# Kernel tuning notes

Hardware: AMD Instinct MI355X
Metric: run time of the kernel (lower is better)

The kernel has to match this reference:

```python
import jax, jax.numpy as jnp
from jax import lax
import numpy as np

H = 128          # hidden_dim
VOCAB = 200000   # word_dim
L = 32           # words per node
NUM_LEAVES = 2048
NUM_PARENTS = 2047
MAXC = 4         # max child slots in a tree row
NCLASS = 4


def setup_inputs() -> dict:
    key = jax.random.key(0)
    ks = jax.random.split(key, 16)
    N = NUM_LEAVES + NUM_PARENTS
    x_word = jax.random.uniform(ks[0], (N, L), dtype=jnp.float32)
    x_index = jax.random.randint(ks[1], (N, L), 0, VOCAB)
    # caterpillar tree: parent idx has one leaf child and the previous parent
    idx = np.arange(NUM_PARENTS)
    tree = np.full((NUM_PARENTS, MAXC), -1, dtype=np.int32)
    tree[:, 0] = idx
    tree[:, 1] = np.where(idx > 0, NUM_LEAVES + idx - 1, NUM_LEAVES - 1)
    tree = jnp.asarray(tree)
    y = jax.random.uniform(ks[2], (NCLASS,), dtype=jnp.float32)
    def init(k, shp):
        return 0.1 * jax.random.normal(k, shp, dtype=jnp.float32)
    return dict(
        x_word=x_word, x_index=x_index, tree=tree, y=y,
        E_bu=init(ks[3], (H, VOCAB)),
        WQ=init(ks[4], (H, H)), WK=init(ks[5], (H, H)), WV=init(ks[6], (H, H)),
        W_z=init(ks[7], (H, H)), U_z=init(ks[8], (H, H)), b_z=jnp.zeros((H,), jnp.float32),
        W_r=init(ks[9], (H, H)), U_r=init(ks[10], (H, H)), b_r=jnp.zeros((H,), jnp.float32),
        W_h=init(ks[11], (H, H)), U_h=init(ks[12], (H, H)), b_h=jnp.zeros((H,), jnp.float32),
        W_out=init(ks[13], (NCLASS, H)), b_out=jnp.zeros((NCLASS,), jnp.float32),
    )


def _forward(x_word, y, E_bu, WQ, WK, WV, W_z, U_z, b_z, W_r, U_r, b_r,
             W_h, U_h, b_h, W_out, b_out, x_index, tree):
    Hd = E_bu.shape[0]
    # parent_xe for every node: weighted sum of embedding columns  [N, H]
    emb = E_bu.T[x_index]                        # [N, L, H] gather
    xe = jnp.einsum('nlh,nl->nh', emb, x_word)
    n_parents = tree.shape[0]
    n_leaves = x_word.shape[0] - n_parents

    def cell(xe_i, h_tilde):
        # W.mul(v).sum(dim=1) == W @ v in the torch code
        z = jax.nn.sigmoid(W_z @ xe_i + U_z @ h_tilde + b_z)
        r = jax.nn.sigmoid(W_r @ xe_i + U_r @ h_tilde + b_r)
        c = jnp.tanh(W_h @ xe_i + U_h @ (h_tilde * r) + b_h)
        return z * h_tilde + (1.0 - z) * c

    # leaves: child_h == 0  =>  h_tilde == 0 (vectorized over all leaves)
    xe_leaf = xe[:n_leaves]
    z_l = jax.nn.sigmoid(xe_leaf @ W_z.T + b_z)
    c_l = jnp.tanh(xe_leaf @ W_h.T + b_h)
    leaf_h = (1.0 - z_l) * c_l

    node_h0 = jnp.zeros((x_word.shape[0], Hd), xe.dtype).at[:n_leaves].set(leaf_h)
    scale = 1.0 / jnp.sqrt(jnp.asarray(Hd, xe.dtype))

    def step(node_h, inp):
        xe_p, row, i = inp
        mask = row >= 0
        child_h = node_h[jnp.clip(row, 0)]                  # [MAXC, H]
        query = jax.nn.sigmoid(xe_p @ WQ)                   # sigmoid(xe @ WQ)
        keyv = child_h @ WK
        val = child_h @ WV
        scores = jnp.where(mask, (query * scale * keyv).sum(-1), -1e9)
        attn = jax.nn.softmax(scores)                       # over children
        h_tilde = attn @ val
        h = cell(xe_p, h_tilde)
        return node_h.at[i].set(h), h

    idxs = jnp.arange(n_parents) + n_leaves
    _, parent_hs = lax.scan(step, node_h0, (xe[n_leaves:], tree, idxs))
    root = parent_hs[-1]
    pred = jax.nn.softmax(W_out @ root + b_out)
    loss = jnp.sum((y - pred) ** 2)
    return pred, loss


def reference(x_word, x_index, tree, y, E_bu, WQ, WK, WV, W_z, U_z, b_z,
              W_r, U_r, b_r, W_h, U_h, b_h, W_out, b_out):
    return _forward(x_word, y, E_bu, WQ, WK, WV, W_z, U_z, b_z, W_r, U_r, b_r,
                    W_h, U_h, b_h, W_out, b_out, x_index, tree)
```

## Files before the change

### kernel.cpp

```cpp
#include <hip/hip_runtime.h>
#include <math.h>

#define HD 128
#define LW 32
#define VOCABN 200000
#define NLEAF 2048
#define NPAR 2047
#define NNODE 4095
#define MAXC 4
#define NCLASS 4
#define SCALE 0.08838834764831845f

#define OFF_XE   0
#define OFF_NODE 524160
#define OFF_W3   786304
#define OFF_WQ   851840
#define OFF_AZ   1113856
#define OFF_AR   1375872
#define OFF_AH   1637888
#define OFF_PREV 1899904
#define OFF_ES   2685952
#define OFF_HG   2688000
#define OFF_HTR  2688128
#define OFF_ET   2688256
#define WS_END   (OFF_ET + (size_t)VOCABN * HD)

#define BARL() asm volatile("s_waitcnt lgkmcnt(0)\n\ts_barrier" ::: "memory")
#define PIN4(v) asm volatile("" : "+v"((v).x), "+v"((v).y), "+v"((v).z), "+v"((v).w))
#define LD4(p, k) (*(const float4*)((p) + 4 * (k)))

#define PIN_ALL() do { PIN4(A0); PIN4(A1); PIN4(A2); PIN4(A3); \
    PIN4(A4); PIN4(A5); PIN4(A6); PIN4(A7); PIN4(A8); PIN4(A9); \
    PIN4(A10); PIN4(A11); PIN4(A12); PIN4(A13); PIN4(A14); PIN4(A15); } while (0)

#define CHRL(W, B) { \
    float s0_ = __int_as_float(__builtin_amdgcn_readlane(xi_, (B) + 0)); \
    float s1_ = __int_as_float(__builtin_amdgcn_readlane(xi_, (B) + 1)); \
    float s2_ = __int_as_float(__builtin_amdgcn_readlane(xi_, (B) + 2)); \
    float s3_ = __int_as_float(__builtin_amdgcn_readlane(xi_, (B) + 3)); \
    a0 += (W).x * s0_ + (W).y * s1_; a1 += (W).z * s2_ + (W).w * s3_; }

#define MATVEC_RL() do { \
    CHRL(A0, 0)   CHRL(A1, 4)   CHRL(A2, 8)   CHRL(A3, 12) \
    CHRL(A4, 16)  CHRL(A5, 20)  CHRL(A6, 24)  CHRL(A7, 28) \
    CHRL(A8, 32)  CHRL(A9, 36)  CHRL(A10, 40) CHRL(A11, 44) \
    CHRL(A12, 48) CHRL(A13, 52) CHRL(A14, 56) CHRL(A15, 60) } while (0)

__global__ void k_xe(const float* __restrict__ xw, const int* __restrict__ xi,
                     const float* __restrict__ E, float* __restrict__ xe) {
    int n = blockIdx.x;
    int h = threadIdx.x;
    __shared__ int   sidx[LW];
    __shared__ float sw[LW];
    if (h < LW) { sidx[h] = xi[n * LW + h]; sw[h] = xw[n * LW + h]; }
    __syncthreads();
    float acc = 0.f;
#pragma unroll
    for (int l = 0; l < LW; ++l)
        acc += E[(size_t)h * VOCABN + sidx[l]] * sw[l];
    xe[(size_t)n * HD + h] = acc;
}

__global__ void k_transpose(const float* __restrict__ E, float* __restrict__ ET) {
    __shared__ float tile[32][33];
    int vb = blockIdx.x * 32, hb = blockIdx.y * 32;
    int tx = threadIdx.x, ty = threadIdx.y;
#pragma unroll
    for (int r = 0; r < 32; r += 8)
        tile[ty + r][tx] = E[(size_t)(hb + ty + r) * VOCABN + vb + tx];
    __syncthreads();
#pragma unroll
    for (int r = 0; r < 32; r += 8)
        ET[(size_t)(vb + ty + r) * HD + hb + tx] = tile[tx][ty + r];
}

__global__ void k_xe_t(const float* __restrict__ xw, const int* __restrict__ xi,
                       const float* __restrict__ ET, float* __restrict__ xe) {
    int n = blockIdx.x;
    int h = threadIdx.x;
    __shared__ int   sidx[LW];
    __shared__ float sw[LW];
    if (h < LW) { sidx[h] = xi[n * LW + h]; sw[h] = xw[n * LW + h]; }
    __syncthreads();
    float acc = 0.f;
#pragma unroll
    for (int l = 0; l < LW; ++l)
        acc += ET[(size_t)sidx[l] * HD + h] * sw[l];
    xe[(size_t)n * HD + h] = acc;
}

__global__ void k_leaf(const float* __restrict__ xe, const float* __restrict__ Wz,
                       const float* __restrict__ bz, const float* __restrict__ Wh,
                       const float* __restrict__ bh, float* __restrict__ node_h) {
    int n = blockIdx.x;
    int j = threadIdx.x;
    __shared__ float xl[HD];
    xl[j] = xe[(size_t)n * HD + j];
    __syncthreads();
    float az = bz[j], ah = bh[j];
    const float* wzr = Wz + (size_t)j * HD;
    const float* whr = Wh + (size_t)j * HD;
#pragma unroll 4
    for (int k = 0; k < HD; ++k) { az += wzr[k] * xl[k]; ah += whr[k] * xl[k]; }
    float z = 1.f / (1.f + expf(-az));
    float c = tanhf(ah);
    node_h[(size_t)n * HD + j] = (1.f - z) * c;
}

__global__ void k_fuse(const float* __restrict__ WV, const float* __restrict__ Uz,
                       const float* __restrict__ Ur, const float* __restrict__ Uh,
                       float* __restrict__ w3) {
    int r = blockIdx.x;
    int b = threadIdx.x;
    float v;
    if (r < 128) {
        v = WV[(size_t)b * HD + r];
    } else if (r < 384) {
        const float* u  = (r < 256 ? Uz + (size_t)(r - 128) * HD : Ur + (size_t)(r - 256) * HD);
        const float* wv = WV + (size_t)b * HD;
        float a = 0.f;
#pragma unroll 4
        for (int j = 0; j < HD; ++j) a += u[j] * wv[j];
        v = a;
    } else {
        v = Uh[(size_t)(r - 384) * HD + b];
    }
    w3[(size_t)r * HD + b] = v;
}

__global__ void k_ppre(const float* __restrict__ xe, const float* __restrict__ WQ,
                       const float* __restrict__ WK, const float* __restrict__ Wz,
                       const float* __restrict__ bz, const float* __restrict__ Wr,
                       const float* __restrict__ br, const float* __restrict__ Wh,
                       const float* __restrict__ bh, float* __restrict__ wq,
                       float* __restrict__ az, float* __restrict__ ar,
                       float* __restrict__ ah) {
    int i = blockIdx.x;
    int j = threadIdx.x;
    __shared__ float xl[HD], ql[HD];
    xl[j] = xe[(size_t)(NLEAF + i) * HD + j];
    __syncthreads();
    float q = 0.f;
#pragma unroll 4
    for (int h = 0; h < HD; ++h) q += xl[h] * WQ[(size_t)h * HD + j];
    ql[j] = 1.f / (1.f + expf(-q));
    __syncthreads();
    float w = 0.f;
#pragma unroll 4
    for (int k = 0; k < HD; ++k) w += WK[(size_t)j * HD + k] * ql[k];
    wq[(size_t)i * HD + j] = w;
    float vz = bz[j], vr = br[j], vh = bh[j];
#pragma unroll 4
    for (int k = 0; k < HD; ++k) {
        float xv = xl[k];
        vz += Wz[(size_t)j * HD + k] * xv;
        vr += Wr[(size_t)j * HD + k] * xv;
        vh += Wh[(size_t)j * HD + k] * xv;
    }
    az[(size_t)i * HD + j] = vz;
    ar[(size_t)i * HD + j] = vr;
    ah[(size_t)i * HD + j] = vh;
}

__global__ void k_chpre(const int* __restrict__ tree, const float* __restrict__ node_h,
                        const float* __restrict__ w3, const float* __restrict__ wq_all,
                        float* __restrict__ preVexp, float* __restrict__ expsum) {
    int i = blockIdx.x;
    int j = threadIdx.x;
    __shared__ float hl[HD];
    __shared__ float red[HD];
    float wqj = wq_all[(size_t)i * HD + j];
    float acc0 = 0.f, acc1 = 0.f, acc2 = 0.f, esum = 0.f;
    for (int c = 0; c < MAXC; ++c) {
        int child = tree[i * MAXC + c];
        if (child < 0 || child >= NLEAF) continue;
        __syncthreads();
        hl[j] = node_h[(size_t)child * HD + j];
        __syncthreads();
        red[j] = hl[j] * wqj;
        __syncthreads();
        for (int s = 64; s > 0; s >>= 1) {
            if (j < s) red[j] += red[j + s];
            __syncthreads();
        }
        float e = expf(red[0] * SCALE);
        float d0 = 0.f, d1 = 0.f, d2 = 0.f;
#pragma unroll 4
        for (int k = 0; k < HD; ++k) {
            float x = hl[k];
            d0 += w3[(size_t)j * HD + k] * x;
            d1 += w3[(size_t)(128 + j) * HD + k] * x;
            d2 += w3[(size_t)(256 + j) * HD + k] * x;
        }
        acc0 += e * d0; acc1 += e * d1; acc2 += e * d2; esum += e;
    }
    preVexp[(size_t)i * 384 + j]       = acc0;
    preVexp[(size_t)i * 384 + 128 + j] = acc1;
    preVexp[(size_t)i * 384 + 256 + j] = acc2;
    if (j == 0) expsum[i] = esum;
}

__global__ __launch_bounds__(1024)
__attribute__((amdgpu_waves_per_eu(4, 4)))
void k_seq(float* __restrict__ ws, const float* __restrict__ Wout,
           const float* __restrict__ bout, const float* __restrict__ y,
           float* __restrict__ out) {
    const int t  = threadIdx.x;
    const int l  = t & 63;
    const int w  = t >> 6;
    const bool isP1 = (w < 12);
    const int q1   = w & 1;
    const int row1 = 64 * (w >> 1) + l;
    const int w12  = w - 12;
    const int q3   = w12 & 1;
    const int row3 = 64 * (w12 >> 1) + l;
    const int q    = isP1 ? q1 : q3;
    const int m    = 64 * q + l;

    __shared__ float part1[768];
    __shared__ float part3[256];
    __shared__ float red[HD];
    __shared__ float sScore;
    __shared__ float hfin[HD];
    __shared__ float outv[NCLASS];

    const int woff = isP1 ? (row1 * HD + 64 * q1)
                          : ((384 + row3) * HD + 64 * q3);
    const float* wp = ws + OFF_W3 + woff;
    float4 A0 = LD4(wp, 0),  A1 = LD4(wp, 1),  A2 = LD4(wp, 2),  A3 = LD4(wp, 3),
           A4 = LD4(wp, 4),  A5 = LD4(wp, 5),  A6 = LD4(wp, 6),  A7 = LD4(wp, 7),
           A8 = LD4(wp, 8),  A9 = LD4(wp, 9),  A10 = LD4(wp, 10), A11 = LD4(wp, 11),
           A12 = LD4(wp, 12), A13 = LD4(wp, 13), A14 = LD4(wp, 14), A15 = LD4(wp, 15);
    PIN_ALL();

    float pv0 = ws[OFF_PREV + m];
    float pv1 = ws[OFF_PREV + 128 + m];
    float pv2 = ws[OFF_PREV + 256 + m];
    float paz = ws[OFF_AZ + m];
    float par = ws[OFF_AR + m];
    float pah = ws[OFF_AH + m];
    float pes = ws[OFF_ES];
    float pwq = ws[OFF_WQ + HD + m];

    float h_lane = 0.f;
    if (t < HD) red[t] = (t < 64) ? -1e30f : 0.f;
    __syncthreads();

    float zreg = 0.f, htvreg = 0.f;

    for (int i = 0; i < NPAR; ++i) {
        const int inext = (i + 1 < NPAR) ? i + 1 : NPAR - 1;
        const int in2   = (i + 2 < NPAR) ? i + 2 : NPAR - 1;

        PIN_ALL();

        if (isP1) {
            const int xi_ = __float_as_int(h_lane);
            float a0 = 0.f, a1 = 0.f;
            MATVEC_RL();
            part1[q1 * 384 + row1] = a0 + a1;
        } else if (w == 12) {
            float s = red[l] + red[l + 64];
#pragma unroll
            for (int o = 32; o > 0; o >>= 1) s += __shfl_down(s, o, 64);
            if (l == 0) sScore = s * SCALE;
        }
        BARL();

        {
            float sc  = sScore;
            float e   = expf(sc);
            float vd  = part1[m]       + part1[384 + m];
            float zd  = part1[128 + m] + part1[512 + m];
            float rd  = part1[256 + m] + part1[640 + m];
            float inv = 1.f / (pes + e);
            float htv = (pv0 + e * vd) * inv;
            float z   = 1.f / (1.f + expf(-(paz + (pv1 + e * zd) * inv)));
            float rr  = 1.f / (1.f + expf(-(par + (pv2 + e * rd) * inv)));
            float htr = htv * rr;
            zreg = z; htvreg = htv;
            if (!isP1) {
                const int xi_ = __float_as_int(htr);
                float a0 = 0.f, a1 = 0.f;
                MATVEC_RL();
                part3[q3 * 128 + row3] = a0 + a1;
            }
        }
        BARL();

        {
            float u  = part3[m] + part3[128 + m];
            float c  = tanhf(pah + u);
            float hv = zreg * htvreg + (1.f - zreg) * c;
            h_lane = hv;
            if (w < 2) red[m] = hv * pwq;
        }
        pv0 = ws[OFF_PREV + inext * 384 + m];
        pv1 = ws[OFF_PREV + inext * 384 + 128 + m];
        pv2 = ws[OFF_PREV + inext * 384 + 256 + m];
        paz = ws[OFF_AZ + inext * HD + m];
        par = ws[OFF_AR + inext * HD + m];
        pah = ws[OFF_AH + inext * HD + m];
        pes = ws[OFF_ES + inext];
        pwq = ws[OFF_WQ + in2 * HD + m];
        BARL();
    }

    if (w < 2) hfin[m] = h_lane;
    __syncthreads();
    if (t < NCLASS) {
        float acc = bout[t];
#pragma unroll 4
        for (int k = 0; k < HD; ++k) acc += Wout[(size_t)t * HD + k] * hfin[k];
        outv[t] = acc;
    }
    __syncthreads();
    if (t == 0) {
        float mx = fmaxf(fmaxf(outv[0], outv[1]), fmaxf(outv[2], outv[3]));
        float e0 = expf(outv[0] - mx), e1 = expf(outv[1] - mx);
        float e2 = expf(outv[2] - mx), e3 = expf(outv[3] - mx);
        float inv = 1.f / (e0 + e1 + e2 + e3);
        float p0 = e0 * inv, p1 = e1 * inv, p2 = e2 * inv, p3 = e3 * inv;
        out[0] = p0; out[1] = p1; out[2] = p2; out[3] = p3;
        float d0 = y[0] - p0, d1 = y[1] - p1, d2 = y[2] - p2, d3 = y[3] - p3;
        out[4] = d0 * d0 + d1 * d1 + d2 * d2 + d3 * d3;
    }
}

extern "C" void kernel_launch(void* const* d_in, const int* in_sizes, int n_in,
                              void* d_out, int out_size, void* d_ws, size_t ws_size,
                              hipStream_t stream) {
    const float* x_word  = (const float*)d_in[0];
    const int*   x_index = (const int*)d_in[1];
    const int*   tree    = (const int*)d_in[2];
    const float* y       = (const float*)d_in[3];
    const float* E_bu    = (const float*)d_in[4];
    const float* WQ      = (const float*)d_in[5];
    const float* WK      = (const float*)d_in[6];
    const float* WV      = (const float*)d_in[7];
    const float* W_z     = (const float*)d_in[8];
    const float* U_z     = (const float*)d_in[9];
    const float* b_z     = (const float*)d_in[10];
    const float* W_r     = (const float*)d_in[11];
    const float* U_r     = (const float*)d_in[12];
    const float* b_r     = (const float*)d_in[13];
    const float* W_h     = (const float*)d_in[14];
    const float* U_h     = (const float*)d_in[15];
    const float* b_h     = (const float*)d_in[16];
    const float* W_out   = (const float*)d_in[17];
    const float* b_out   = (const float*)d_in[18];

    float* ws      = (float*)d_ws;
    float* xe      = ws + OFF_XE;
    float* node_h  = ws + OFF_NODE;
    float* w3      = ws + OFF_W3;
    float* wq      = ws + OFF_WQ;
    float* az      = ws + OFF_AZ;
    float* ar      = ws + OFF_AR;
    float* ah      = ws + OFF_AH;
    float* preVexp = ws + OFF_PREV;
    float* expsum  = ws + OFF_ES;
    float* ET      = ws + OFF_ET;

    bool use_transpose = ws_size >= WS_END * sizeof(float);

    if (use_transpose) {
        dim3 tg(VOCABN / 32, HD / 32), tb(32, 8);
        k_transpose<<<tg, tb, 0, stream>>>(E_bu, ET);
        k_xe_t<<<NNODE, HD, 0, stream>>>(x_word, x_index, ET, xe);
    } else {
        k_xe<<<NNODE, HD, 0, stream>>>(x_word, x_index, E_bu, xe);
    }
    k_leaf<<<NLEAF, HD, 0, stream>>>(xe, W_z, b_z, W_h, b_h, node_h);
    k_fuse<<<512, HD, 0, stream>>>(WV, U_z, U_r, U_h, w3);
    k_ppre<<<NPAR, HD, 0, stream>>>(xe, WQ, WK, W_z, b_z, W_r, b_r, W_h, b_h,
                                    wq, az, ar, ah);
    k_chpre<<<NPAR, HD, 0, stream>>>(tree, node_h, w3, wq, preVexp, expsum);
    k_seq<<<1, 1024, 0, stream>>>(ws, W_out, b_out, y, (float*)d_out);
}
```

Measured before the change: 4.412 ms.

## Repartition sequential matvecs into 32-column chunks with two rows per lane

Changes how the 16 waves split the per-step matrix-vector products. Each wave now covers a 32-column slice and two output rows, so it issues half as many readlanes per FMA and has twice the independent accumulators. The input vector goes through LDS (h_lds) instead of a per-lane register, and only the last four waves run the gate and elementwise work. Partial sums are now reduced over four chunks instead of two, which adds LDS reads and traffic on the serial critical path.

```diff
diff --git a/kernel.cpp b/kernel.cpp
--- a/kernel.cpp
+++ b/kernel.cpp
@@ -33,18 +33,19 @@
     PIN4(A4); PIN4(A5); PIN4(A6); PIN4(A7); PIN4(A8); PIN4(A9); \
     PIN4(A10); PIN4(A11); PIN4(A12); PIN4(A13); PIN4(A14); PIN4(A15); } while (0)
 
-#define CHRL(W, B) { \
-    float s0_ = __int_as_float(__builtin_amdgcn_readlane(xi_, (B) + 0)); \
-    float s1_ = __int_as_float(__builtin_amdgcn_readlane(xi_, (B) + 1)); \
-    float s2_ = __int_as_float(__builtin_amdgcn_readlane(xi_, (B) + 2)); \
-    float s3_ = __int_as_float(__builtin_amdgcn_readlane(xi_, (B) + 3)); \
-    a0 += (W).x * s0_ + (W).y * s1_; a1 += (W).z * s2_ + (W).w * s3_; }
-
-#define MATVEC_RL() do { \
-    CHRL(A0, 0)   CHRL(A1, 4)   CHRL(A2, 8)   CHRL(A3, 12) \
-    CHRL(A4, 16)  CHRL(A5, 20)  CHRL(A6, 24)  CHRL(A7, 28) \
-    CHRL(A8, 32)  CHRL(A9, 36)  CHRL(A10, 40) CHRL(A11, 44) \
-    CHRL(A12, 48) CHRL(A13, 52) CHRL(A14, 56) CHRL(A15, 60) } while (0)
+#define RL(x, j) __int_as_float(__builtin_amdgcn_readlane((x), (j)))
+
+#define CH2(WA, WB, XS, J) { \
+    float s0_ = RL(XS, (J) + 0), s1_ = RL(XS, (J) + 1); \
+    float s2_ = RL(XS, (J) + 2), s3_ = RL(XS, (J) + 3); \
+    a0 += (WA).x * s0_ + (WA).y * s1_; a1 += (WA).z * s2_ + (WA).w * s3_; \
+    b0 += (WB).x * s0_ + (WB).y * s1_; b1 += (WB).z * s2_ + (WB).w * s3_; }
+
+#define MATVEC2(XS, BASE) do { \
+    CH2(A0, A8,  XS, (BASE) + 0)  CH2(A1, A9,  XS, (BASE) + 4)  \
+    CH2(A2, A10, XS, (BASE) + 8)  CH2(A3, A11, XS, (BASE) + 12) \
+    CH2(A4, A12, XS, (BASE) + 16) CH2(A5, A13, XS, (BASE) + 20) \
+    CH2(A6, A14, XS, (BASE) + 24) CH2(A7, A15, XS, (BASE) + 28) } while (0)
 
 __global__ void k_xe(const float* __restrict__ xw, const int* __restrict__ xi,
                      const float* __restrict__ E, float* __restrict__ xe) {
@@ -209,41 +210,45 @@
     const int l  = t & 63;
     const int w  = t >> 6;
     const bool isP1 = (w < 12);
-    const int q1   = w & 1;
-    const int row1 = 64 * (w >> 1) + l;
-    const int w12  = w - 12;
-    const int q3   = w12 & 1;
-    const int row3 = 64 * (w12 >> 1) + l;
-    const int q    = isP1 ? q1 : q3;
-    const int m    = 64 * q + l;
-
-    __shared__ float part1[768];
-    __shared__ float part3[256];
+    const int c1 = w & 3;
+    const int g1 = w >> 2;
+    const int r0 = 128 * g1 + l;
+    const int w12 = w - 12;
+    const int c3  = w12 & 3;
+    const int q3  = c3 >> 1;
+    const int m3  = 64 * q3 + l;
+
+    __shared__ float part1[4 * 384];
+    __shared__ float part3[4 * 128];
     __shared__ float red[HD];
-    __shared__ float sScore;
-    __shared__ float hfin[HD];
+    __shared__ float sS;
+    __shared__ float h_lds[HD];
     __shared__ float outv[NCLASS];
 
-    const int woff = isP1 ? (row1 * HD + 64 * q1)
-                          : ((384 + row3) * HD + 64 * q3);
-    const float* wp = ws + OFF_W3 + woff;
-    float4 A0 = LD4(wp, 0),  A1 = LD4(wp, 1),  A2 = LD4(wp, 2),  A3 = LD4(wp, 3),
-           A4 = LD4(wp, 4),  A5 = LD4(wp, 5),  A6 = LD4(wp, 6),  A7 = LD4(wp, 7),
-           A8 = LD4(wp, 8),  A9 = LD4(wp, 9),  A10 = LD4(wp, 10), A11 = LD4(wp, 11),
-           A12 = LD4(wp, 12), A13 = LD4(wp, 13), A14 = LD4(wp, 14), A15 = LD4(wp, 15);
+    const int woff = isP1 ? (r0 * HD + 32 * c1)
+                          : ((384 + l) * HD + 32 * c3);
+    const float* wp0 = ws + OFF_W3 + woff;
+    const float* wp1 = wp0 + 64 * HD;
+    float4 A0 = LD4(wp0, 0), A1 = LD4(wp0, 1), A2 = LD4(wp0, 2), A3 = LD4(wp0, 3),
+           A4 = LD4(wp0, 4), A5 = LD4(wp0, 5), A6 = LD4(wp0, 6), A7 = LD4(wp0, 7),
+           A8 = LD4(wp1, 0), A9 = LD4(wp1, 1), A10 = LD4(wp1, 2), A11 = LD4(wp1, 3),
+           A12 = LD4(wp1, 4), A13 = LD4(wp1, 5), A14 = LD4(wp1, 6), A15 = LD4(wp1, 7);
     PIN_ALL();
 
-    float pv0 = ws[OFF_PREV + m];
-    float pv1 = ws[OFF_PREV + 128 + m];
-    float pv2 = ws[OFF_PREV + 256 + m];
-    float paz = ws[OFF_AZ + m];
-    float par = ws[OFF_AR + m];
-    float pah = ws[OFF_AH + m];
-    float pes = ws[OFF_ES];
-    float pwq = ws[OFF_WQ + HD + m];
-
-    float h_lane = 0.f;
-    if (t < HD) red[t] = (t < 64) ? -1e30f : 0.f;
+    float pv0 = 0.f, pv1 = 0.f, pv2 = 0.f, paz = 0.f, par = 0.f, pah = 0.f,
+          pwq = 0.f, pes = 0.f;
+    if (!isP1) {
+        pv0 = ws[OFF_PREV + m3];       pv1 = ws[OFF_PREV + 128 + m3];
+        pv2 = ws[OFF_PREV + 256 + m3];
+        paz = ws[OFF_AZ + m3];         par = ws[OFF_AR + m3];
+        pah = ws[OFF_AH + m3];
+        pes = ws[OFF_ES];
+        pwq = ws[OFF_WQ + HD + m3];
+    }
+    if (t < HD) {
+        h_lds[t] = 0.f;
+        red[t]   = (t < 64) ? -1e30f : 0.f;
+    }
     __syncthreads();
 
     float zreg = 0.f, htvreg = 0.f;
@@ -255,63 +260,66 @@
         PIN_ALL();
 
         if (isP1) {
-            const int xi_ = __float_as_int(h_lane);
-            float a0 = 0.f, a1 = 0.f;
-            MATVEC_RL();
-            part1[q1 * 384 + row1] = a0 + a1;
-        } else if (w == 12) {
+            const int hx = __float_as_int(h_lds[32 * c1 + (l & 31)]);
+            float a0 = 0.f, a1 = 0.f, b0 = 0.f, b1 = 0.f;
+            MATVEC2(hx, 0);
+            part1[c1 * 384 + r0]      = a0 + a1;
+            part1[c1 * 384 + r0 + 64] = b0 + b1;
+        } else if (w12 == 0) {
             float s = red[l] + red[l + 64];
 #pragma unroll
             for (int o = 32; o > 0; o >>= 1) s += __shfl_down(s, o, 64);
-            if (l == 0) sScore = s * SCALE;
+            if (l == 0) sS = s * SCALE;
         }
         BARL();
 
-        {
-            float sc  = sScore;
-            float e   = expf(sc);
-            float vd  = part1[m]       + part1[384 + m];
-            float zd  = part1[128 + m] + part1[512 + m];
-            float rd  = part1[256 + m] + part1[640 + m];
+        if (!isP1) {
+            float e   = expf(sS);
+            float vd  = part1[m3]        + part1[384 + m3]
+                      + part1[768 + m3]  + part1[1152 + m3];
+            float zd  = part1[128 + m3]  + part1[512 + m3]
+                      + part1[896 + m3]  + part1[1280 + m3];
+            float rd  = part1[256 + m3]  + part1[640 + m3]
+                      + part1[1024 + m3] + part1[1408 + m3];
             float inv = 1.f / (pes + e);
             float htv = (pv0 + e * vd) * inv;
             float z   = 1.f / (1.f + expf(-(paz + (pv1 + e * zd) * inv)));
             float rr  = 1.f / (1.f + expf(-(par + (pv2 + e * rd) * inv)));
             float htr = htv * rr;
             zreg = z; htvreg = htv;
-            if (!isP1) {
-                const int xi_ = __float_as_int(htr);
-                float a0 = 0.f, a1 = 0.f;
-                MATVEC_RL();
-                part3[q3 * 128 + row3] = a0 + a1;
-            }
+            const int xh = __float_as_int(htr);
+            float a0 = 0.f, a1 = 0.f, b0 = 0.f, b1 = 0.f;
+            if ((c3 & 1) == 0) { MATVEC2(xh, 0); } else { MATVEC2(xh, 32); }
+            part3[c3 * 128 + l]      = a0 + a1;
+            part3[c3 * 128 + l + 64] = b0 + b1;
         }
         BARL();
 
-        {
-            float u  = part3[m] + part3[128 + m];
+        if (!isP1) {
+            float u  = part3[m3]       + part3[128 + m3]
+                     + part3[256 + m3] + part3[384 + m3];
             float c  = tanhf(pah + u);
             float hv = zreg * htvreg + (1.f - zreg) * c;
-            h_lane = hv;
-            if (w < 2) red[m] = hv * pwq;
-        }
-        pv0 = ws[OFF_PREV + inext * 384 + m];
-        pv1 = ws[OFF_PREV + inext * 384 + 128 + m];
-        pv2 = ws[OFF_PREV + inext * 384 + 256 + m];
-        paz = ws[OFF_AZ + inext * HD + m];
-        par = ws[OFF_AR + inext * HD + m];
-        pah = ws[OFF_AH + inext * HD + m];
-        pes = ws[OFF_ES + inext];
-        pwq = ws[OFF_WQ + in2 * HD + m];
+            if ((w12 & 1) == 0) {
+                h_lds[m3] = hv;
+                red[m3]   = hv * pwq;
+            }
+            pv0 = ws[OFF_PREV + inext * 384 + m3];
+            pv1 = ws[OFF_PREV + inext * 384 + 128 + m3];
+            pv2 = ws[OFF_PREV + inext * 384 + 256 + m3];
+            paz = ws[OFF_AZ + inext * HD + m3];
+            par = ws[OFF_AR + inext * HD + m3];
+            pah = ws[OFF_AH + inext * HD + m3];
+            pes = ws[OFF_ES + inext];
+            pwq = ws[OFF_WQ + in2 * HD + m3];
+        }
         BARL();
     }
 
-    if (w < 2) hfin[m] = h_lane;
-    __syncthreads();
     if (t < NCLASS) {
         float acc = bout[t];
 #pragma unroll 4
-        for (int k = 0; k < HD; ++k) acc += Wout[(size_t)t * HD + k] * hfin[k];
+        for (int k = 0; k < HD; ++k) acc += Wout[(size_t)t * HD + k] * h_lds[k];
         outv[t] = acc;
     }
     __syncthreads();
```

Result: faster. 3.663 ms, median of 2 (-17.0%).
